# Optimization experiments

Hardware: AMD Instinct MI355X
Metric: run time of the kernel (lower is better)

## Reference

```python
import jax, jax.numpy as jnp
import numpy as np

N_SRC = 50000
N_DST = 50000
E = 800000
F_IN = 128
H = 4
D = 32
NEG_SLOPE = 0.2


def setup_inputs() -> dict:
    key = jax.random.key(0)
    k1, k2, k3, k4, k5, k6, k7, k8 = jax.random.split(key, 8)
    src_feat = jax.random.normal(k1, (N_SRC, F_IN), dtype=jnp.float32)
    dst_feat = jax.random.normal(k2, (N_DST, F_IN), dtype=jnp.float32)
    edge_feat = jax.random.normal(k3, (E, F_IN), dtype=jnp.float32)
    src_idx = jax.random.randint(k4, (E,), 0, N_SRC, dtype=jnp.int32)
    dst_idx = jax.random.randint(k5, (E,), 0, N_DST, dtype=jnp.int32)
    # fc_src: in = 2*F_IN (concat op), out = H*D; fc_dst: in = F_IN, out = H*D
    g = np.sqrt(2.0)  # gain for 'relu' (xavier_normal_)
    W_src = jax.random.normal(k6, (2 * F_IN, H * D), dtype=jnp.float32) * (g * np.sqrt(2.0 / (2 * F_IN + H * D)))
    W_dst = jax.random.normal(k7, (F_IN, H * D), dtype=jnp.float32) * (g * np.sqrt(2.0 / (F_IN + H * D)))
    bias = jnp.zeros((H * D,), dtype=jnp.float32)
    return {"src_feat": src_feat, "dst_feat": dst_feat, "edge_feat": edge_feat,
            "W_src": W_src, "W_dst": W_dst, "bias": bias,
            "src_idx": src_idx, "dst_idx": dst_idx}


def reference(src_feat, dst_feat, edge_feat, W_src, W_dst, bias, src_idx, dst_idx):
    # Per-edge message: concat(src[e], edge[e]) @ W_src -> [E, H, D]
    m = jnp.concatenate([src_feat[src_idx], edge_feat], axis=1) @ W_src
    m = m.reshape(E, H, D)
    # Destination projection: [N_dst, H, D]
    nh = (dst_feat @ W_dst).reshape(N_DST, H, D)
    # e_add_v then LeakyReLU -> attention logits [E, H, D]
    scores = jax.nn.leaky_relu(m + nh[dst_idx], negative_slope=NEG_SLOPE)
    # edge_softmax: segment softmax over edges incident to each destination,
    # computed independently per (head, out_feat) channel.
    mx = jax.ops.segment_max(scores, dst_idx, num_segments=N_DST)
    ex = jnp.exp(scores - mx[dst_idx])
    denom = jax.ops.segment_sum(ex, dst_idx, num_segments=N_DST)
    attn = ex / denom[dst_idx]
    # Weighted scatter-add aggregation -> [N_dst, H, D]
    rst = jax.ops.segment_sum(m * attn, dst_idx, num_segments=N_DST)
    rst = rst + bias.reshape(1, H, D)
    return rst
```

## Files before the change

kernel.cpp:

```cpp
#include <hip/hip_runtime.h>


#define F 128
#define C 128
#define NEG 0.2f
#define NN 50000
#define EE 800000

__device__ __forceinline__ void fma4(float4& a, float s, const float4 w) {
    a.x += s * w.x; a.y += s * w.y; a.z += s * w.z; a.w += s * w.w;
}

__global__ __launch_bounds__(256) void node_proj_kernel(
    const float* __restrict__ src_feat, const float* __restrict__ dst_feat,
    const float* __restrict__ W_src, const float* __restrict__ W_dst,
    float* __restrict__ src_proj, float* __restrict__ nh)
{
    const float* in; const float* W; float* out;
    if (blockIdx.y == 0) { in = src_feat; W = W_src; out = src_proj; }
    else                 { in = dst_feat; W = W_dst; out = nh; }

    __shared__ float4 xs[8 * 32];
    const int t  = threadIdx.x;
    const int nb = blockIdx.x * 8;

    {
        int row = t >> 5, col = t & 31;
        xs[t] = ((const float4*)(in + (size_t)(nb + row) * F))[col];
    }
    __syncthreads();

    const int jq = t & 31;
    const int ng = t >> 5;
    float4 acc = make_float4(0.f, 0.f, 0.f, 0.f);
    const float4* W4 = (const float4*)W;

    #pragma unroll 4
    for (int k4 = 0; k4 < 32; ++k4) {
        float4 xv = xs[ng * 32 + k4];
        float4 w0 = W4[(4 * k4 + 0) * 32 + jq];
        float4 w1 = W4[(4 * k4 + 1) * 32 + jq];
        float4 w2 = W4[(4 * k4 + 2) * 32 + jq];
        float4 w3 = W4[(4 * k4 + 3) * 32 + jq];
        fma4(acc, xv.x, w0); fma4(acc, xv.y, w1);
        fma4(acc, xv.z, w2); fma4(acc, xv.w, w3);
    }
    ((float4*)(out + (size_t)(nb + ng) * C))[jq] = acc;
}

__global__ __launch_bounds__(256) void hist_kernel(
    const int* __restrict__ dst_idx, int* __restrict__ deg)
{
    int e = blockIdx.x * 256 + threadIdx.x;
    if (e < EE) atomicAdd(&deg[dst_idx[e]], 1);
}

__global__ __launch_bounds__(1024) void scan_kernel(
    const int* __restrict__ deg, int* __restrict__ cursor)
{
    __shared__ int ssum[1024];
    const int t = threadIdx.x;
    const int chunk = (NN + 1023) / 1024;
    int lo = t * chunk, hi = lo + chunk; if (hi > NN) hi = NN; if (lo > NN) lo = NN;
    int s = 0;
    for (int i = lo; i < hi; ++i) s += deg[i];
    ssum[t] = s;
    __syncthreads();
    for (int d = 1; d < 1024; d <<= 1) {
        int v = (t >= d) ? ssum[t - d] : 0;
        __syncthreads();
        ssum[t] += v;
        __syncthreads();
    }
    int run = ssum[t] - s;
    for (int i = lo; i < hi; ++i) { cursor[i] = run; run += deg[i]; }
}

__global__ __launch_bounds__(256) void scatter_kernel(
    const int* __restrict__ dst_idx, int* __restrict__ cursor, int* __restrict__ elist)
{
    int e = blockIdx.x * 256 + threadIdx.x;
    if (e < EE) {
        int p = atomicAdd(&cursor[dst_idx[e]], 1);
        elist[p] = e;
    }
}

__global__ __launch_bounds__(256) void edge_kernel(
    const float* __restrict__ edge_feat, const float* __restrict__ Wb,
    const float* __restrict__ src_proj, const float* __restrict__ nh,
    const int* __restrict__ src_idx, const int* __restrict__ dst_idx,
    const int* __restrict__ elist,
    float* __restrict__ num, float* __restrict__ den)
{
    __shared__ float4 xs[64 * 32];
    __shared__ int sidx[64];
    __shared__ int didx[64];
    __shared__ int es[64];

    const int t  = threadIdx.x;
    const int eb = blockIdx.x * 64;

    if (t < 64) {
        int e = elist[eb + t];
        es[t] = e;
        sidx[t] = src_idx[e];
        didx[t] = dst_idx[e];
    }
    __syncthreads();

    #pragma unroll
    for (int i = 0; i < 8; ++i) {
        int flat = t + i * 256;
        int row = flat >> 5, col = flat & 31;
        xs[flat] = ((const float4*)(edge_feat + (size_t)es[row] * F))[col];
    }
    __syncthreads();

    const int jq = t & 31;
    const int eg = t >> 5;

    float4 acc[8];
    #pragma unroll
    for (int i = 0; i < 8; ++i) acc[i] = make_float4(0.f, 0.f, 0.f, 0.f);

    const float4* W4 = (const float4*)Wb;

    #pragma unroll 2
    for (int k4 = 0; k4 < 32; ++k4) {
        float4 w0 = W4[(4 * k4 + 0) * 32 + jq];
        float4 w1 = W4[(4 * k4 + 1) * 32 + jq];
        float4 w2 = W4[(4 * k4 + 2) * 32 + jq];
        float4 w3 = W4[(4 * k4 + 3) * 32 + jq];
        #pragma unroll
        for (int i = 0; i < 8; ++i) {
            float4 xv = xs[(eg * 8 + i) * 32 + k4];
            fma4(acc[i], xv.x, w0); fma4(acc[i], xv.y, w1);
            fma4(acc[i], xv.z, w2); fma4(acc[i], xv.w, w3);
        }
    }

    int cur = didx[eg * 8];
    float4 nv = ((const float4*)(nh + (size_t)cur * C))[jq];
    float4 nacc = make_float4(0.f, 0.f, 0.f, 0.f);
    float4 dacc = make_float4(0.f, 0.f, 0.f, 0.f);

    #pragma unroll
    for (int i = 0; i < 8; ++i) {
        int el = eg * 8 + i;
        int d  = didx[el];
        if (d != cur) {
            float* np = num + (size_t)cur * C + jq * 4;
            float* dp = den + (size_t)cur * C + jq * 4;
            atomicAdd(np + 0, nacc.x); atomicAdd(np + 1, nacc.y);
            atomicAdd(np + 2, nacc.z); atomicAdd(np + 3, nacc.w);
            atomicAdd(dp + 0, dacc.x); atomicAdd(dp + 1, dacc.y);
            atomicAdd(dp + 2, dacc.z); atomicAdd(dp + 3, dacc.w);
            nacc = make_float4(0.f, 0.f, 0.f, 0.f);
            dacc = make_float4(0.f, 0.f, 0.f, 0.f);
            cur = d;
            nv = ((const float4*)(nh + (size_t)d * C))[jq];
        }
        float4 sp = ((const float4*)(src_proj + (size_t)sidx[el] * C))[jq];

        float m0 = acc[i].x + sp.x, m1 = acc[i].y + sp.y;
        float m2 = acc[i].z + sp.z, m3 = acc[i].w + sp.w;

        float s0 = m0 + nv.x, s1 = m1 + nv.y, s2 = m2 + nv.z, s3 = m3 + nv.w;
        s0 = s0 > 0.f ? s0 : NEG * s0;
        s1 = s1 > 0.f ? s1 : NEG * s1;
        s2 = s2 > 0.f ? s2 : NEG * s2;
        s3 = s3 > 0.f ? s3 : NEG * s3;

        float e0 = __expf(s0), e1 = __expf(s1), e2 = __expf(s2), e3 = __expf(s3);

        nacc.x += e0 * m0; nacc.y += e1 * m1; nacc.z += e2 * m2; nacc.w += e3 * m3;
        dacc.x += e0;      dacc.y += e1;      dacc.z += e2;      dacc.w += e3;
    }
    {
        float* np = num + (size_t)cur * C + jq * 4;
        float* dp = den + (size_t)cur * C + jq * 4;
        atomicAdd(np + 0, nacc.x); atomicAdd(np + 1, nacc.y);
        atomicAdd(np + 2, nacc.z); atomicAdd(np + 3, nacc.w);
        atomicAdd(dp + 0, dacc.x); atomicAdd(dp + 1, dacc.y);
        atomicAdd(dp + 2, dacc.z); atomicAdd(dp + 3, dacc.w);
    }
}

__global__ __launch_bounds__(256) void finalize_kernel(
    const float* __restrict__ num, const float* __restrict__ den,
    const float* __restrict__ bias, float* __restrict__ out)
{
    int i = blockIdx.x * 256 + threadIdx.x;
    float4 n = ((const float4*)num)[i];
    float4 d = ((const float4*)den)[i];
    float4 b = ((const float4*)bias)[i & 31];
    float4 r;
    r.x = (d.x != 0.f ? n.x / d.x : 0.f) + b.x;
    r.y = (d.y != 0.f ? n.y / d.y : 0.f) + b.y;
    r.z = (d.z != 0.f ? n.z / d.z : 0.f) + b.z;
    r.w = (d.w != 0.f ? n.w / d.w : 0.f) + b.w;
    ((float4*)out)[i] = r;
}

extern "C" void kernel_launch(void* const* d_in, const int* in_sizes, int n_in,
                              void* d_out, int out_size, void* d_ws, size_t ws_size,
                              hipStream_t stream) {
    const float* src_feat  = (const float*)d_in[0];
    const float* dst_feat  = (const float*)d_in[1];
    const float* edge_feat = (const float*)d_in[2];
    const float* W_src     = (const float*)d_in[3];
    const float* W_dst     = (const float*)d_in[4];
    const float* bias      = (const float*)d_in[5];
    const int*   src_idx   = (const int*)d_in[6];
    const int*   dst_idx   = (const int*)d_in[7];
    float* out = (float*)d_out;

    const size_t NODEF = (size_t)NN * C;

    float* ws       = (float*)d_ws;
    float* src_proj = ws;
    float* nh       = ws + NODEF;
    float* den      = ws + 2 * NODEF;
    int*   deg      = (int*)(ws + 3 * NODEF);
    int*   cursor   = deg + NN;
    int*   elist    = cursor + NN;

    float* num = out;

    hipMemsetAsync(num, 0, NODEF * sizeof(float), stream);
    hipMemsetAsync(den, 0, NODEF * sizeof(float), stream);
    hipMemsetAsync(deg, 0, NN * sizeof(int), stream);

    hist_kernel<<<(EE + 255) / 256, 256, 0, stream>>>(dst_idx, deg);
    scan_kernel<<<1, 1024, 0, stream>>>(deg, cursor);
    scatter_kernel<<<(EE + 255) / 256, 256, 0, stream>>>(dst_idx, cursor, elist);

    node_proj_kernel<<<dim3(NN / 8, 2), 256, 0, stream>>>(
        src_feat, dst_feat, W_src, W_dst, src_proj, nh);

    edge_kernel<<<EE / 64, 256, 0, stream>>>(
        edge_feat, W_src + 128 * 128, src_proj, nh, src_idx, dst_idx, elist, num, den);

    finalize_kernel<<<NODEF / 4 / 256, 256, 0, stream>>>(num, den, bias, out);
}
```

Measured before the change: 1.397 ms.

## Compute edge-feature projection with fp16 MFMA using pre-swizzled weight fragments

Replaces the scalar fp32 FMA loop for the edge_feat @ W_src[128:] product with MFMA 16x16x32 f16 instructions. A new prep kernel converts the bottom half of W_src to fp16 in MFMA B-fragment order. Edge features are converted to fp16 into XOR-swizzled LDS, and the results are staged back through LDS for the existing softmax/scatter epilogue. This removes the FP32 ALU bottleneck in the edge kernel, at the cost of fp16 rounding of inputs and weights, higher LDS usage (48KB) and an extra launch.

After: 1.422 ms. About the same (+1.8%).

```diff
diff --git a/kernel.cpp b/kernel.cpp
--- a/kernel.cpp
+++ b/kernel.cpp
@@ -6,6 +6,9 @@
 #define NEG 0.2f
 #define NN 50000
 #define EE 800000
+
+typedef _Float16 half8 __attribute__((ext_vector_type(8)));
+typedef float f32x4 __attribute__((ext_vector_type(4)));
 
 __device__ __forceinline__ void fma4(float4& a, float s, const float4 w) {
     a.x += s * w.x; a.y += s * w.y; a.z += s * w.z; a.w += s * w.w;
@@ -86,14 +89,27 @@
     }
 }
 
+__global__ __launch_bounds__(256) void prep_w_kernel(
+    const float* __restrict__ W_src, _Float16* __restrict__ bfrag)
+{
+    int i = blockIdx.x * 256 + threadIdx.x;
+    int j  = i & 7;
+    int lw = (i >> 3) & 63;
+    int ks = (i >> 9) & 3;
+    int ct = i >> 11;
+    int k  = ks * 32 + (lw >> 4) * 8 + j;
+    int ch = ct * 16 + (lw & 15);
+    bfrag[i] = (_Float16)W_src[(size_t)(128 + k) * 128 + ch];
+}
+
 __global__ __launch_bounds__(256) void edge_kernel(
-    const float* __restrict__ edge_feat, const float* __restrict__ Wb,
+    const float* __restrict__ edge_feat, const _Float16* __restrict__ bfrag,
     const float* __restrict__ src_proj, const float* __restrict__ nh,
     const int* __restrict__ src_idx, const int* __restrict__ dst_idx,
     const int* __restrict__ elist,
     float* __restrict__ num, float* __restrict__ den)
 {
-    __shared__ float4 xs[64 * 32];
+    __shared__ __align__(16) unsigned char smem[49152];
     __shared__ int sidx[64];
     __shared__ int didx[64];
     __shared__ int es[64];
@@ -109,36 +125,62 @@
     }
     __syncthreads();
 
-    #pragma unroll
-    for (int i = 0; i < 8; ++i) {
+    {
+        const float4* bg = (const float4*)bfrag;
+        float4* bl = (float4*)(smem + 16384);
+        #pragma unroll
+        for (int i = 0; i < 8; ++i) bl[i * 256 + t] = bg[i * 256 + t];
+    }
+
+    #pragma unroll
+    for (int i = 0; i < 4; ++i) {
         int flat = t + i * 256;
-        int row = flat >> 5, col = flat & 31;
-        xs[flat] = ((const float4*)(edge_feat + (size_t)es[row] * F))[col];
+        int r = flat >> 4, c = flat & 15;
+        const float4* row = (const float4*)(edge_feat + (size_t)es[r] * F);
+        float4 f0 = row[2 * c], f1 = row[2 * c + 1];
+        half8 h;
+        h[0] = (_Float16)f0.x; h[1] = (_Float16)f0.y;
+        h[2] = (_Float16)f0.z; h[3] = (_Float16)f0.w;
+        h[4] = (_Float16)f1.x; h[5] = (_Float16)f1.y;
+        h[6] = (_Float16)f1.z; h[7] = (_Float16)f1.w;
+        *(half8*)(smem + (r << 8) + ((c ^ (r & 7)) << 4)) = h;
+    }
+    __syncthreads();
+
+    const int l  = t & 63;
+    const int w  = t >> 6;
+    const int er = l & 15;
+    const int g  = l >> 4;
+    f32x4 acc[8];
+    {
+        f32x4 z = {0.f, 0.f, 0.f, 0.f};
+        #pragma unroll
+        for (int ct = 0; ct < 8; ++ct) acc[ct] = z;
+    }
+    #pragma unroll
+    for (int ks = 0; ks < 4; ++ks) {
+        half8 a = *(const half8*)(smem + ((w * 16 + er) << 8)
+                                       + ((((ks << 2) + g) ^ (er & 7)) << 4));
+        #pragma unroll
+        for (int ct = 0; ct < 8; ++ct) {
+            half8 b = *(const half8*)(smem + 16384 + ((((ct << 2) + ks) << 6) + l) * 16);
+            acc[ct] = __builtin_amdgcn_mfma_f32_16x16x32_f16(a, b, acc[ct], 0, 0, 0);
+        }
+    }
+    __syncthreads();
+
+    float* m_lds = (float*)smem;
+    #pragma unroll
+    for (int ct = 0; ct < 8; ++ct) {
+        #pragma unroll
+        for (int rg = 0; rg < 4; ++rg) {
+            m_lds[(w * 16 + g * 4 + rg) * 128 + ct * 16 + er] = acc[ct][rg];
+        }
     }
     __syncthreads();
 
     const int jq = t & 31;
     const int eg = t >> 5;
-
-    float4 acc[8];
-    #pragma unroll
-    for (int i = 0; i < 8; ++i) acc[i] = make_float4(0.f, 0.f, 0.f, 0.f);
-
-    const float4* W4 = (const float4*)Wb;
-
-    #pragma unroll 2
-    for (int k4 = 0; k4 < 32; ++k4) {
-        float4 w0 = W4[(4 * k4 + 0) * 32 + jq];
-        float4 w1 = W4[(4 * k4 + 1) * 32 + jq];
-        float4 w2 = W4[(4 * k4 + 2) * 32 + jq];
-        float4 w3 = W4[(4 * k4 + 3) * 32 + jq];
-        #pragma unroll
-        for (int i = 0; i < 8; ++i) {
-            float4 xv = xs[(eg * 8 + i) * 32 + k4];
-            fma4(acc[i], xv.x, w0); fma4(acc[i], xv.y, w1);
-            fma4(acc[i], xv.z, w2); fma4(acc[i], xv.w, w3);
-        }
-    }
 
     int cur = didx[eg * 8];
     float4 nv = ((const float4*)(nh + (size_t)cur * C))[jq];
@@ -161,10 +203,11 @@
             cur = d;
             nv = ((const float4*)(nh + (size_t)d * C))[jq];
         }
+        float4 mi = *(const float4*)(m_lds + el * 128 + jq * 4);
         float4 sp = ((const float4*)(src_proj + (size_t)sidx[el] * C))[jq];
 
-        float m0 = acc[i].x + sp.x, m1 = acc[i].y + sp.y;
-        float m2 = acc[i].z + sp.z, m3 = acc[i].w + sp.w;
+        float m0 = mi.x + sp.x, m1 = mi.y + sp.y;
+        float m2 = mi.z + sp.z, m3 = mi.w + sp.w;
 
         float s0 = m0 + nv.x, s1 = m1 + nv.y, s2 = m2 + nv.z, s3 = m3 + nv.w;
         s0 = s0 > 0.f ? s0 : NEG * s0;
@@ -225,6 +268,7 @@
     int*   deg      = (int*)(ws + 3 * NODEF);
     int*   cursor   = deg + NN;
     int*   elist    = cursor + NN;
+    _Float16* bfrag = (_Float16*)(elist + EE);
 
     float* num = out;
 
@@ -236,11 +280,13 @@
     scan_kernel<<<1, 1024, 0, stream>>>(deg, cursor);
     scatter_kernel<<<(EE + 255) / 256, 256, 0, stream>>>(dst_idx, cursor, elist);
 
+    prep_w_kernel<<<64, 256, 0, stream>>>(W_src, bfrag);
+
     node_proj_kernel<<<dim3(NN / 8, 2), 256, 0, stream>>>(
         src_feat, dst_feat, W_src, W_dst, src_proj, nh);
 
     edge_kernel<<<EE / 64, 256, 0, stream>>>(
-        edge_feat, W_src + 128 * 128, src_proj, nh, src_idx, dst_idx, elist, num, den);
+        edge_feat, bfrag, src_proj, nh, src_idx, dst_idx, elist, num, den);
 
     finalize_kernel<<<NODEF / 4 / 256, 256, 0, stream>>>(num, den, bias, out);
 }
```
